# Optimization experiments

Hardware: AMD Instinct MI355X
Metric: run time of the kernel (lower is better)

## Reference

```python
import jax, jax.numpy as jnp
import numpy as np

SEQ_LEN = 30
H_DIM = 64
EMB = 16
N_SAMPLES = 3
TRAJ_PTS = N_SAMPLES * 2  # 6
BATCH = 131072


def setup_inputs() -> dict:
    key = jax.random.key(0)
    ks = jax.random.split(key, 16)
    s = 0.05
    return {
        "traj_abs": jax.random.normal(ks[0], (1, BATCH, 2), jnp.float32),
        "traj_rel": jax.random.normal(ks[1], (1, BATCH, 2), jnp.float32),
        "h0": jax.random.normal(ks[2], (1, BATCH, H_DIM), jnp.float32),
        "c0": jax.random.normal(ks[3], (1, BATCH, H_DIM), jnp.float32),
        # LSTM weights (PyTorch layout: gates ordered i, f, g, o)
        "W_ih": jax.random.normal(ks[4], (4 * H_DIM, EMB), jnp.float32) * s,
        "W_hh": jax.random.normal(ks[5], (4 * H_DIM, H_DIM), jnp.float32) * s,
        "b_ih": jax.random.normal(ks[6], (4 * H_DIM,), jnp.float32) * s,
        "b_hh": jax.random.normal(ks[7], (4 * H_DIM,), jnp.float32) * s,
        # spatial_embedding: Linear(6 -> 16)
        "W_se": jax.random.normal(ks[8], (EMB, TRAJ_PTS), jnp.float32) * s,
        "b_se": jax.random.normal(ks[9], (EMB,), jnp.float32) * s,
        # hidden2pos: Linear(64 -> 6)
        "W_h2p": jax.random.normal(ks[10], (TRAJ_PTS, H_DIM), jnp.float32) * s,
        "b_h2p": jax.random.normal(ks[11], (TRAJ_PTS,), jnp.float32) * s,
        # confidences: Linear(64 -> 3)
        "W_conf": jax.random.normal(ks[12], (N_SAMPLES, H_DIM), jnp.float32) * s,
        "b_conf": jax.random.normal(ks[13], (N_SAMPLES,), jnp.float32) * s,
    }


def reference(traj_abs, traj_rel, h0, c0, W_ih, W_hh, b_ih, b_hh,
              W_se, b_se, W_h2p, b_h2p, W_conf, b_conf):
    b = traj_rel.shape[1]
    # repeat_interleave of (x,y) pairs n_samples times -> [x,y,x,y,x,y]
    traj6 = jnp.tile(traj_rel[0], (1, N_SAMPLES))            # (b, 6)
    x = jax.nn.leaky_relu(traj6 @ W_se.T + b_se)             # (b, 16)
    h = h0[0]                                                # (b, 64)
    c = c0[0]

    def step(carry, _):
        h, c, x = carry
        gates = x @ W_ih.T + h @ W_hh.T + (b_ih + b_hh)      # (b, 256)
        i, f, g, o = jnp.split(gates, 4, axis=-1)
        i = jax.nn.sigmoid(i)
        f = jax.nn.sigmoid(f)
        g = jnp.tanh(g)
        o = jax.nn.sigmoid(o)
        c = f * c + i * g
        h = o * jnp.tanh(c)
        rel = h @ W_h2p.T + b_h2p                            # (b, 6)
        x = jax.nn.leaky_relu(rel @ W_se.T + b_se)           # (b, 16)
        return (h, c, x), rel

    (h, c, x), rels = jax.lax.scan(step, (h, c, x), None, length=SEQ_LEN)
    # rels: (seq_len, b, 6) -> (seq_len, b, n_samples, 2) -> (b, n_samples, seq_len, 2)
    pred = rels.reshape(SEQ_LEN, b, N_SAMPLES, 2).transpose(1, 2, 0, 3)
    conf = jax.nn.softmax(h @ W_conf.T + b_conf, axis=1)     # (b, 3)
    return pred, conf
```

## Files before the change

kernel.cpp:

```cpp
#include <hip/hip_runtime.h>

typedef __bf16 bf16x8 __attribute__((ext_vector_type(8)));
typedef float f32x16 __attribute__((ext_vector_type(16)));
typedef unsigned int uintv2 __attribute__((ext_vector_type(2)));

#define LOG2E 1.44269504088896340736f

static __device__ __forceinline__ unsigned pk2(float a, float b) {
  unsigned short ua = __builtin_bit_cast(unsigned short, (__bf16)a);
  unsigned short ub = __builtin_bit_cast(unsigned short, (__bf16)b);
  return ((unsigned)ub << 16) | (unsigned)ua;
}

static __device__ __forceinline__ float fast_sig(float x) {
  return __builtin_amdgcn_rcpf(1.0f + __builtin_amdgcn_exp2f(-LOG2E * x));
}
static __device__ __forceinline__ float fast_tanh(float x) {
  return 1.0f - 2.0f * __builtin_amdgcn_rcpf(1.0f + __builtin_amdgcn_exp2f((2.0f * LOG2E) * x));
}

static __device__ __forceinline__ f32x16 mfma_bf16(bf16x8 a, bf16x8 b, f32x16 c) {
  return __builtin_amdgcn_mfma_f32_32x32x16_bf16(a, b, c, 0, 0, 0);
}
static __device__ __forceinline__ bf16x8 frag_of(uint4 w) {
  return __builtin_bit_cast(bf16x8, w);
}
static __device__ __forceinline__ f32x16 load16(const float* p) {
  const float4 q0 = *(const float4*)(p + 0);
  const float4 q1 = *(const float4*)(p + 4);
  const float4 q2 = *(const float4*)(p + 8);
  const float4 q3 = *(const float4*)(p + 12);
  return (f32x16){q0.x, q0.y, q0.z, q0.w, q1.x, q1.y, q1.z, q1.w,
                  q2.x, q2.y, q2.z, q2.w, q3.x, q3.y, q3.z, q3.w};
}

static __device__ __forceinline__ void build_hfrag(const unsigned hpk[2][8], bf16x8 hfrag[4]) {
#pragma unroll
  for (int ks = 0; ks < 4; ++ks) {
    const int T = ks >> 1, s2 = ks & 1;
    uintv2 ra = __builtin_amdgcn_permlane32_swap(hpk[T][4 * s2 + 0], hpk[T][4 * s2 + 2], false, false);
    uintv2 rb = __builtin_amdgcn_permlane32_swap(hpk[T][4 * s2 + 1], hpk[T][4 * s2 + 3], false, false);
    uint4 w; w.x = ra[0]; w.y = rb[0]; w.z = ra[1]; w.w = rb[1];
    hfrag[ks] = frag_of(w);
  }
}
static __device__ __forceinline__ bf16x8 build_xfrag(const unsigned xpk[4]) {
  uintv2 ra = __builtin_amdgcn_permlane32_swap(xpk[0], xpk[2], false, false);
  uintv2 rb = __builtin_amdgcn_permlane32_swap(xpk[1], xpk[3], false, false);
  uint4 w; w.x = ra[0]; w.y = rb[0]; w.z = ra[1]; w.w = rb[1];
  return frag_of(w);
}

static __device__ __forceinline__ f32x16 gate_acc(const uint4* s_frag, int m, int lane,
                                                  const bf16x8 hfrag[4], bf16x8 xfrag,
                                                  f32x16 acc) {
#pragma unroll
  for (int ks = 0; ks < 4; ++ks)
    acc = mfma_bf16(frag_of(s_frag[(m * 5 + ks) * 64 + lane]), hfrag[ks], acc);
  acc = mfma_bf16(frag_of(s_frag[(m * 5 + 4) * 64 + lane]), xfrag, acc);
  return acc;
}

template <bool USE_WS>
__global__ __launch_bounds__(256, 1)
void mmdec_kernel(const float* __restrict__ traj_rel,
                  const float* __restrict__ h0p, const float* __restrict__ c0p,
                  const float* __restrict__ W_ih, const float* __restrict__ W_hh,
                  const float* __restrict__ b_ih, const float* __restrict__ b_hh,
                  const float* __restrict__ W_se, const float* __restrict__ b_se,
                  const float* __restrict__ W_h2p, const float* __restrict__ b_h2p,
                  const float* __restrict__ W_conf, const float* __restrict__ b_conf,
                  float* __restrict__ out, float* __restrict__ wsP, int btot)
{
  __shared__ uint4 s_frag[49 * 64];
  __shared__ __align__(16) float s_gb[256];
  __shared__ __align__(16) float s_rb[32];
  __shared__ __align__(16) float s_xb[32];
  __shared__ __align__(16) float s_cb[32];

  const int tid  = threadIdx.x;
  const int lane = tid & 63;
  const int wid  = tid >> 6;
  const int hi   = lane >> 5;
  const int col  = lane & 31;

  if (wid == 0) {
    for (int m = 0; m < 8; ++m) {
      for (int ks = 0; ks < 5; ++ks) {
        const int row = m * 32 + col;
        const float* p = (ks < 4) ? (W_hh + row * 64 + ks * 16 + hi * 8)
                                  : (W_ih + row * 16 + hi * 8);
        uint4 w;
        w.x = pk2(p[0], p[1]); w.y = pk2(p[2], p[3]);
        w.z = pk2(p[4], p[5]); w.w = pk2(p[6], p[7]);
        s_frag[(m * 5 + ks) * 64 + lane] = w;
      }
    }
    for (int ks = 0; ks < 4; ++ks) {
      float f[8];
      for (int e = 0; e < 8; ++e)
        f[e] = (col < 6) ? W_h2p[col * 64 + ks * 16 + hi * 8 + e] : 0.f;
      uint4 w; w.x = pk2(f[0], f[1]); w.y = pk2(f[2], f[3]);
      w.z = pk2(f[4], f[5]); w.w = pk2(f[6], f[7]);
      s_frag[(40 + ks) * 64 + lane] = w;
    }
    {
      float f[8];
      for (int e = 0; e < 8; ++e) {
        const int k = hi * 8 + e;
        f[e] = (col < 16 && k < 6) ? W_se[col * 6 + k] : 0.f;
      }
      uint4 w; w.x = pk2(f[0], f[1]); w.y = pk2(f[2], f[3]);
      w.z = pk2(f[4], f[5]); w.w = pk2(f[6], f[7]);
      s_frag[44 * 64 + lane] = w;
    }
    for (int ks = 0; ks < 4; ++ks) {
      float f[8];
      for (int e = 0; e < 8; ++e)
        f[e] = (col < 3) ? W_conf[col * 64 + ks * 16 + hi * 8 + e] : 0.f;
      uint4 w; w.x = pk2(f[0], f[1]); w.y = pk2(f[2], f[3]);
      w.z = pk2(f[4], f[5]); w.w = pk2(f[6], f[7]);
      s_frag[(45 + ks) * 64 + lane] = w;
    }
  }
  {
    const int r = tid & 15;
    if (tid < 256) {
      const int bh = tid >> 7, m = (tid >> 4) & 7;
      const int row = m * 32 + (r & 3) + ((r >> 2) << 3) + bh * 4;
      s_gb[tid] = b_ih[row] + b_hh[row];
    }
    if (tid < 32) {
      const int bh = tid >> 4;
      const int row = (r & 3) + ((r >> 2) << 3) + bh * 4;
      s_rb[tid] = (row < 6)  ? b_h2p[row]  : 0.f;
      s_xb[tid] = (row < 16) ? b_se[row]   : 0.f;
      s_cb[tid] = (row < 3)  ? b_conf[row] : 0.f;
    }
  }
  __syncthreads();

  const int batch = (blockIdx.x * 4 + wid) * 32 + col;
  float cst[2][16];
  unsigned hpk[2][8];
  bf16x8 hfrag[4];
  bf16x8 xfrag;

  {
    float hv[2][16];
#pragma unroll
    for (int T = 0; T < 2; ++T) {
#pragma unroll
      for (int q = 0; q < 4; ++q) {
        const float4 h4 = *(const float4*)(h0p + (long)batch * 64 + T * 32 + q * 8 + hi * 4);
        const float4 c4 = *(const float4*)(c0p + (long)batch * 64 + T * 32 + q * 8 + hi * 4);
        hv[T][q * 4 + 0] = h4.x; hv[T][q * 4 + 1] = h4.y; hv[T][q * 4 + 2] = h4.z; hv[T][q * 4 + 3] = h4.w;
        cst[T][q * 4 + 0] = c4.x; cst[T][q * 4 + 1] = c4.y; cst[T][q * 4 + 2] = c4.z; cst[T][q * 4 + 3] = c4.w;
      }
    }
#pragma unroll
    for (int T = 0; T < 2; ++T)
#pragma unroll
      for (int j = 0; j < 8; ++j)
        hpk[T][j] = pk2(hv[T][2 * j], hv[T][2 * j + 1]);
    build_hfrag(hpk, hfrag);
  }
  {
    const float tx = traj_rel[(long)batch * 2 + 0];
    const float ty = traj_rel[(long)batch * 2 + 1];
    unsigned xpk[4];
#pragma unroll
    for (int j = 0; j < 4; ++j) {
      float vv[2];
#pragma unroll
      for (int u = 0; u < 2; ++u) {
        const int r = 2 * j + u;
        const int row = (r & 3) + ((r >> 2) << 3) + hi * 4;
        const float a0 = W_se[row * 6 + 0] + W_se[row * 6 + 2] + W_se[row * 6 + 4];
        const float a1 = W_se[row * 6 + 1] + W_se[row * 6 + 3] + W_se[row * 6 + 5];
        const float v = tx * a0 + ty * a1 + b_se[row];
        vv[u] = (v >= 0.f) ? v : 0.01f * v;
      }
      xpk[j] = pk2(vv[0], vv[1]);
    }
    xfrag = build_xfrag(xpk);
  }

  float* outP = out + (long)batch * 180;
  float* outC = out + (long)btot * 180 + (long)batch * 3;

#pragma unroll 1
  for (int t = 0; t < 30; ++t) {
#pragma unroll
    for (int T = 0; T < 2; ++T) {
      f32x16 ag = gate_acc(s_frag, 4 + T, lane, hfrag, xfrag,
                           load16(s_gb + hi * 128 + (4 + T) * 16));
      __builtin_amdgcn_sched_barrier(0);
      {
        f32x16 ai = gate_acc(s_frag, 0 + T, lane, hfrag, xfrag,
                             load16(s_gb + hi * 128 + (0 + T) * 16));
#pragma unroll
        for (int r = 0; r < 16; ++r)
          ag[r] = fast_sig(ai[r]) * fast_tanh(ag[r]);
      }
      __builtin_amdgcn_sched_barrier(0);
      {
        f32x16 af = gate_acc(s_frag, 2 + T, lane, hfrag, xfrag,
                             load16(s_gb + hi * 128 + (2 + T) * 16));
#pragma unroll
        for (int r = 0; r < 16; ++r)
          cst[T][r] = fast_sig(af[r]) * cst[T][r] + ag[r];
      }
      __builtin_amdgcn_sched_barrier(0);
      {
        f32x16 ao = gate_acc(s_frag, 6 + T, lane, hfrag, xfrag,
                             load16(s_gb + hi * 128 + (6 + T) * 16));
#pragma unroll
        for (int j = 0; j < 8; ++j) {
          const float h0v = fast_sig(ao[2 * j])     * fast_tanh(cst[T][2 * j]);
          const float h1v = fast_sig(ao[2 * j + 1]) * fast_tanh(cst[T][2 * j + 1]);
          hpk[T][j] = pk2(h0v, h1v);
        }
      }
      __builtin_amdgcn_sched_barrier(0);
    }
    build_hfrag(hpk, hfrag);

    f32x16 racc = load16(s_rb + hi * 16);
#pragma unroll
    for (int ks = 0; ks < 4; ++ks)
      racc = mfma_bf16(frag_of(s_frag[(40 + ks) * 64 + lane]), hfrag[ks], racc);

    if (USE_WS) {
      if (hi == 0) {
        float2 v0; v0.x = racc[0]; v0.y = racc[1];
        float2 v1; v1.x = racc[2]; v1.y = racc[3];
        *(float2*)(wsP + ((long)(0 * 30 + t) * btot + batch) * 2) = v0;
        *(float2*)(wsP + ((long)(1 * 30 + t) * btot + batch) * 2) = v1;
      } else {
        float2 v2; v2.x = racc[0]; v2.y = racc[1];
        *(float2*)(wsP + ((long)(2 * 30 + t) * btot + batch) * 2) = v2;
      }
    } else {
      if (hi == 0) {
        float2 v0; v0.x = racc[0]; v0.y = racc[1];
        float2 v1; v1.x = racc[2]; v1.y = racc[3];
        *(float2*)(outP + t * 2)       = v0;
        *(float2*)(outP + 60 + t * 2)  = v1;
      } else {
        float2 v2; v2.x = racc[0]; v2.y = racc[1];
        *(float2*)(outP + 120 + t * 2) = v2;
      }
    }

    {
      const unsigned qw = pk2(racc[0], racc[1]);
      const unsigned pw = pk2(racc[2], racc[3]);
      uintv2 sw = __builtin_amdgcn_permlane32_swap(qw, 0u, false, false);
      uint4 rw; rw.x = sw[0]; rw.y = pw; rw.z = sw[1]; rw.w = 0u;
      f32x16 xacc = load16(s_xb + hi * 16);
      xacc = mfma_bf16(frag_of(s_frag[44 * 64 + lane]), frag_of(rw), xacc);
      unsigned xpk[4];
#pragma unroll
      for (int j = 0; j < 4; ++j) {
        float v0 = xacc[2 * j], v1 = xacc[2 * j + 1];
        v0 = (v0 >= 0.f) ? v0 : 0.01f * v0;
        v1 = (v1 >= 0.f) ? v1 : 0.01f * v1;
        xpk[j] = pk2(v0, v1);
      }
      xfrag = build_xfrag(xpk);
    }
  }

  {
    f32x16 cacc = load16(s_cb + hi * 16);
#pragma unroll
    for (int ks = 0; ks < 4; ++ks)
      cacc = mfma_bf16(frag_of(s_frag[(45 + ks) * 64 + lane]), hfrag[ks], cacc);
    if (hi == 0) {
      const float a = cacc[0], b = cacc[1], c = cacc[2];
      const float mx = fmaxf(a, fmaxf(b, c));
      const float e0 = __builtin_amdgcn_exp2f(LOG2E * (a - mx));
      const float e1 = __builtin_amdgcn_exp2f(LOG2E * (b - mx));
      const float e2 = __builtin_amdgcn_exp2f(LOG2E * (c - mx));
      const float rs = __builtin_amdgcn_rcpf(e0 + e1 + e2);
      outC[0] = e0 * rs; outC[1] = e1 * rs; outC[2] = e2 * rs;
    }
  }
}

__global__ __launch_bounds__(256)
void transpose_pred(const float* __restrict__ ws, float* __restrict__ out, int btot)
{
  __shared__ float s_t[64][188];
  const int tid = threadIdx.x;
  const long b0 = (long)blockIdx.x * 64;

#pragma unroll 1
  for (int i = 0; i < 23; ++i) {
    const int idx = tid + i * 256;
    if (idx < 5760) {
      const int e = idx >> 6, bb = idx & 63;
      const float2 v = *(const float2*)(ws + ((long)e * btot + b0 + bb) * 2);
      *(float2*)&s_t[bb][e * 2] = v;
    }
  }
  __syncthreads();

#pragma unroll 1
  for (int i = 0; i < 12; ++i) {
    const int idx = tid + i * 256;
    if (idx < 2880) {
      const int b = idx / 45, k = idx % 45;
      *(float4*)(out + (b0 + b) * 180 + k * 4) = *(const float4*)&s_t[b][k * 4];
    }
  }
}

extern "C" void kernel_launch(void* const* d_in, const int* in_sizes, int n_in,
                              void* d_out, int out_size, void* d_ws, size_t ws_size,
                              hipStream_t stream) {
  const float* traj_rel = (const float*)d_in[1];
  const float* h0p    = (const float*)d_in[2];
  const float* c0p    = (const float*)d_in[3];
  const float* W_ih   = (const float*)d_in[4];
  const float* W_hh   = (const float*)d_in[5];
  const float* b_ih   = (const float*)d_in[6];
  const float* b_hh   = (const float*)d_in[7];
  const float* W_se   = (const float*)d_in[8];
  const float* b_se   = (const float*)d_in[9];
  const float* W_h2p  = (const float*)d_in[10];
  const float* b_h2p  = (const float*)d_in[11];
  const float* W_conf = (const float*)d_in[12];
  const float* b_conf = (const float*)d_in[13];

  const int btot = in_sizes[1] / 2;
  const int grid = btot / 128;

  const size_t ws_need = (size_t)90 * (size_t)btot * 2 * sizeof(float);
  if (ws_size >= ws_need) {
    mmdec_kernel<true><<<grid, 256, 0, stream>>>(traj_rel, h0p, c0p, W_ih, W_hh, b_ih, b_hh,
                                                 W_se, b_se, W_h2p, b_h2p, W_conf, b_conf,
                                                 (float*)d_out, (float*)d_ws, btot);
    transpose_pred<<<btot / 64, 256, 0, stream>>>((const float*)d_ws, (float*)d_out, btot);
  } else {
    mmdec_kernel<false><<<grid, 256, 0, stream>>>(traj_rel, h0p, c0p, W_ih, W_hh, b_ih, b_hh,
                                                  W_se, b_se, W_h2p, b_h2p, W_conf, b_conf,
                                                  (float*)d_out, nullptr, btot);
  }
}
```

Baseline: 388.6 us.

## Fold activation exponent scales into gate weights and double block size

Pre-scales the LSTM gate weights and biases by -log2(e) or 2·log2(e), so the MFMA output is the exp2 argument directly. The sigmoid·tanh products are then merged to share a single reciprocal each, which cuts multiplies and rcp calls per element. Separately, blocks grow from 4 to 8 waves (512 threads), halving the grid and the number of times the shared weight fragments are staged. Pre-scaling before bf16 rounding changes the rounding error slightly, and the merged (1+e)(1+e) product can overflow to inf for large pre-activations.

```diff
diff --git a/kernel.cpp b/kernel.cpp
--- a/kernel.cpp
+++ b/kernel.cpp
@@ -10,13 +10,6 @@
   unsigned short ua = __builtin_bit_cast(unsigned short, (__bf16)a);
   unsigned short ub = __builtin_bit_cast(unsigned short, (__bf16)b);
   return ((unsigned)ub << 16) | (unsigned)ua;
-}
-
-static __device__ __forceinline__ float fast_sig(float x) {
-  return __builtin_amdgcn_rcpf(1.0f + __builtin_amdgcn_exp2f(-LOG2E * x));
-}
-static __device__ __forceinline__ float fast_tanh(float x) {
-  return 1.0f - 2.0f * __builtin_amdgcn_rcpf(1.0f + __builtin_amdgcn_exp2f((2.0f * LOG2E) * x));
 }
 
 static __device__ __forceinline__ f32x16 mfma_bf16(bf16x8 a, bf16x8 b, f32x16 c) {
@@ -62,7 +55,7 @@
 }
 
 template <bool USE_WS>
-__global__ __launch_bounds__(256, 1)
+__global__ __launch_bounds__(512, 1)
 void mmdec_kernel(const float* __restrict__ traj_rel,
                   const float* __restrict__ h0p, const float* __restrict__ c0p,
                   const float* __restrict__ W_ih, const float* __restrict__ W_hh,
@@ -86,13 +79,14 @@
 
   if (wid == 0) {
     for (int m = 0; m < 8; ++m) {
+      const float gs = (m == 4 || m == 5) ? (2.0f * LOG2E) : (-LOG2E);
       for (int ks = 0; ks < 5; ++ks) {
         const int row = m * 32 + col;
         const float* p = (ks < 4) ? (W_hh + row * 64 + ks * 16 + hi * 8)
                                   : (W_ih + row * 16 + hi * 8);
         uint4 w;
-        w.x = pk2(p[0], p[1]); w.y = pk2(p[2], p[3]);
-        w.z = pk2(p[4], p[5]); w.w = pk2(p[6], p[7]);
+        w.x = pk2(gs * p[0], gs * p[1]); w.y = pk2(gs * p[2], gs * p[3]);
+        w.z = pk2(gs * p[4], gs * p[5]); w.w = pk2(gs * p[6], gs * p[7]);
         s_frag[(m * 5 + ks) * 64 + lane] = w;
       }
     }
@@ -127,8 +121,9 @@
     const int r = tid & 15;
     if (tid < 256) {
       const int bh = tid >> 7, m = (tid >> 4) & 7;
+      const float gs = (m == 4 || m == 5) ? (2.0f * LOG2E) : (-LOG2E);
       const int row = m * 32 + (r & 3) + ((r >> 2) << 3) + bh * 4;
-      s_gb[tid] = b_ih[row] + b_hh[row];
+      s_gb[tid] = gs * (b_ih[row] + b_hh[row]);
     }
     if (tid < 32) {
       const int bh = tid >> 4;
@@ -140,7 +135,7 @@
   }
   __syncthreads();
 
-  const int batch = (blockIdx.x * 4 + wid) * 32 + col;
+  const int batch = (blockIdx.x * 8 + wid) * 32 + col;
   float cst[2][16];
   unsigned hpk[2][8];
   bf16x8 hfrag[4];
@@ -195,21 +190,29 @@
     for (int T = 0; T < 2; ++T) {
       f32x16 ag = gate_acc(s_frag, 4 + T, lane, hfrag, xfrag,
                            load16(s_gb + hi * 128 + (4 + T) * 16));
+#pragma unroll
+      for (int r = 0; r < 16; ++r)
+        ag[r] = __builtin_amdgcn_exp2f(ag[r]);
       __builtin_amdgcn_sched_barrier(0);
       {
         f32x16 ai = gate_acc(s_frag, 0 + T, lane, hfrag, xfrag,
                              load16(s_gb + hi * 128 + (0 + T) * 16));
 #pragma unroll
-        for (int r = 0; r < 16; ++r)
-          ag[r] = fast_sig(ai[r]) * fast_tanh(ag[r]);
+        for (int r = 0; r < 16; ++r) {
+          const float ei = __builtin_amdgcn_exp2f(ai[r]);
+          const float d  = __builtin_amdgcn_rcpf((1.0f + ei) * (1.0f + ag[r]));
+          ag[r] = (ag[r] - 1.0f) * d;
+        }
       }
       __builtin_amdgcn_sched_barrier(0);
       {
         f32x16 af = gate_acc(s_frag, 2 + T, lane, hfrag, xfrag,
                              load16(s_gb + hi * 128 + (2 + T) * 16));
 #pragma unroll
-        for (int r = 0; r < 16; ++r)
-          cst[T][r] = fast_sig(af[r]) * cst[T][r] + ag[r];
+        for (int r = 0; r < 16; ++r) {
+          const float ef = __builtin_amdgcn_exp2f(af[r]);
+          cst[T][r] = __builtin_amdgcn_rcpf(1.0f + ef) * cst[T][r] + ag[r];
+        }
       }
       __builtin_amdgcn_sched_barrier(0);
       {
@@ -217,9 +220,16 @@
                              load16(s_gb + hi * 128 + (6 + T) * 16));
 #pragma unroll
         for (int j = 0; j < 8; ++j) {
-          const float h0v = fast_sig(ao[2 * j])     * fast_tanh(cst[T][2 * j]);
-          const float h1v = fast_sig(ao[2 * j + 1]) * fast_tanh(cst[T][2 * j + 1]);
-          hpk[T][j] = pk2(h0v, h1v);
+          float hn[2];
+#pragma unroll
+          for (int u = 0; u < 2; ++u) {
+            const int r = 2 * j + u;
+            const float eo = __builtin_amdgcn_exp2f(ao[r]);
+            const float ec = __builtin_amdgcn_exp2f((2.0f * LOG2E) * cst[T][r]);
+            const float d  = __builtin_amdgcn_rcpf((1.0f + eo) * (1.0f + ec));
+            hn[u] = (ec - 1.0f) * d;
+          }
+          hpk[T][j] = pk2(hn[0], hn[1]);
         }
       }
       __builtin_amdgcn_sched_barrier(0);
@@ -335,16 +345,16 @@
   const float* b_conf = (const float*)d_in[13];
 
   const int btot = in_sizes[1] / 2;
-  const int grid = btot / 128;
+  const int grid = btot / 256;
 
   const size_t ws_need = (size_t)90 * (size_t)btot * 2 * sizeof(float);
   if (ws_size >= ws_need) {
-    mmdec_kernel<true><<<grid, 256, 0, stream>>>(traj_rel, h0p, c0p, W_ih, W_hh, b_ih, b_hh,
+    mmdec_kernel<true><<<grid, 512, 0, stream>>>(traj_rel, h0p, c0p, W_ih, W_hh, b_ih, b_hh,
                                                  W_se, b_se, W_h2p, b_h2p, W_conf, b_conf,
                                                  (float*)d_out, (float*)d_ws, btot);
     transpose_pred<<<btot / 64, 256, 0, stream>>>((const float*)d_ws, (float*)d_out, btot);
   } else {
-    mmdec_kernel<false><<<grid, 256, 0, stream>>>(traj_rel, h0p, c0p, W_ih, W_hh, b_ih, b_hh,
+    mmdec_kernel<false><<<grid, 512, 0, stream>>>(traj_rel, h0p, c0p, W_ih, W_hh, b_ih, b_hh,
                                                   W_se, b_se, W_h2p, b_h2p, W_conf, b_conf,
                                                   (float*)d_out, nullptr, btot);
   }
```

New measurement: 339.9 us. 12.5% less time.
